# Kernel tuning notes

Hardware: AMD Instinct MI355X
Metric: run time of the kernel (lower is better)

The kernel has to match this reference:

```python
import jax, jax.numpy as jnp
import numpy as np

B, H, W, C = 8, 64, 64, 256
EPS = 1e-5


def unfold(img, k, p):
    # img: [B, C, Hh, Ww] -> patches [B, C, k*k, Hh*Ww] (torch.nn.Unfold layout)
    b, c, hh, ww = img.shape
    xp = jnp.pad(img, ((0, 0), (0, 0), (p, p), (p, p)))
    pats = jnp.stack([xp[:, :, i:i + hh, j:j + ww]
                      for i in range(k) for j in range(k)], axis=2)
    return pats.reshape(b, c, k * k, hh * ww)


def fold(cols, k, p, hh, ww):
    # cols: [B, C*k*k, hh*ww] -> scatter-add back to [B, C, hh, ww] (torch.nn.Fold)
    b = cols.shape[0]
    c = cols.shape[1] // (k * k)
    pt = cols.reshape(b, c, k, k, hh, ww)
    out = jnp.zeros((b, c, hh + 2 * p, ww + 2 * p), cols.dtype)
    for i in range(k):
        for j in range(k):
            out = out.at[:, :, i:i + hh, j:j + ww].add(pt[:, :, i, j])
    return out[:, :, p:p + hh, p:p + ww]


def maxpool(img, k, p):
    # same-size max pool, stride 1
    return jax.lax.reduce_window(img, -jnp.inf, jax.lax.max,
                                 (1, 1, k, k), (1, 1, 1, 1),
                                 [(0, 0), (0, 0), (p, p), (p, p)])


def setup_inputs() -> dict:
    key = jax.random.key(0)
    ks = jax.random.split(key, 4)
    x = jax.random.normal(ks[0], (B, H, W, C), dtype=jnp.float32)
    Wv = jax.random.normal(ks[1], (C, C), dtype=jnp.float32) * 0.02
    bv = jnp.zeros((C,), jnp.float32)
    Wa = jax.random.normal(ks[2], (C, 81), dtype=jnp.float32) * 0.02
    ba = jnp.zeros((81,), jnp.float32)
    Wfu = jax.random.normal(ks[3], (2 * C, C), dtype=jnp.float32) * 0.02
    bfu = jnp.zeros((C,), jnp.float32)
    gamma = jnp.ones((C,), jnp.float32)
    beta = jnp.zeros((C,), jnp.float32)
    return {"x": x, "Wv": Wv, "bv": bv, "Wa": Wa, "ba": ba,
            "Wfu": Wfu, "bfu": bfu, "gamma": gamma, "beta": beta}


def reference(x, Wv, bv, Wa, ba, Wfu, bfu, gamma, beta):
    b, h, w, c = x.shape
    x3 = x
    # 3x3 windowed attention branch (5x5 branch in source is dead code: its
    # result is overwritten by `x2 = relu(x)` before use).
    v = x @ Wv + bv                                # [B,H,W,C]
    v_img = jnp.transpose(v, (0, 3, 2, 1))         # [B,C,W,H] (H/W swap as in source)
    pats = unfold(v_img, 3, 1)                     # [B,C,9,W*H]
    v3 = jnp.transpose(pats, (0, 3, 2, 1))         # [B,HW,9,C]
    a = (x @ Wa + ba).reshape(b, h * w, 9, 9)
    a = jax.nn.softmax(a, axis=-1)
    y = jnp.einsum('lbpq,lbqc->lbpc'.replace('l', 'n'), a, v3)  # [B,HW,9,C]
    y = jnp.transpose(y, (0, 3, 2, 1)).reshape(b, c * 9, h * w)
    xf = fold(y, 3, 1, h, w)                       # [B,C,H,W]
    xf = jnp.transpose(xf, (0, 3, 2, 1))           # [B,W,H,C]
    xr = jax.nn.relu(xf)
    x_max = jnp.transpose(x3, (0, 3, 2, 1))        # [B,C,W,H]
    m1 = jnp.transpose(maxpool(x_max, 3, 1), (0, 3, 2, 1))  # [B,H,W,C]
    x1 = jax.nn.relu(xr + m1)
    x2 = jax.nn.relu(x1)
    m2 = jnp.transpose(maxpool(x_max, 5, 2), (0, 3, 2, 1))
    x2 = jax.nn.relu(x2 + m2)
    xfu = jnp.concatenate([x1, x2], axis=-1) @ Wfu + bfu
    xfu = jax.nn.relu(xfu)
    out = x3 + xfu                                 # [B,H,W,C]
    # BatchNorm2d (training mode: batch stats) applied on [B,C,W,H]
    img = jnp.transpose(out, (0, 3, 2, 1))
    mean = img.mean(axis=(0, 2, 3), keepdims=True)
    var = img.var(axis=(0, 2, 3), keepdims=True)
    imgn = (img - mean) * jax.lax.rsqrt(var + EPS)
    imgn = imgn * gamma[None, :, None, None] + beta[None, :, None, None]
    return jnp.transpose(imgn, (0, 2, 3, 1))       # [B,W,H,C]
```

## Files before the change

kernel.cpp:

```cpp
#include <hip/hip_runtime.h>
#include <math.h>

#define NLOC 32768
#define CH 256

typedef __attribute__((ext_vector_type(8))) short short8;
typedef __attribute__((ext_vector_type(4))) float floatx4;

__device__ inline unsigned short f2bf(float x) {
  union { float f; unsigned u; } c; c.f = x;
  unsigned r = c.u + 0x7FFFu + ((c.u >> 16) & 1u);
  return (unsigned short)(r >> 16);
}
__device__ inline float bflo(unsigned u) {
  union { unsigned u; float f; } c; c.u = u << 16; return c.f;
}
__device__ inline float bfhi(unsigned u) {
  union { unsigned u; float f; } c; c.u = u & 0xFFFF0000u; return c.f;
}

__device__ __forceinline__ void gl_lds16(const void* g, void* l) {
  __builtin_amdgcn_global_load_lds(
      (const __attribute__((address_space(1))) unsigned int*)g,
      (__attribute__((address_space(3))) unsigned int*)l, 16, 0, 0);
}

__global__ __launch_bounds__(64) void k_pack_w(
    const float* __restrict__ Wv, const float* __restrict__ Wa,
    const float* __restrict__ Wfu, unsigned short* __restrict__ wp) {
  int fid = blockIdx.x;
  int l = threadIdx.x;
  const float* W; int ldn, nvalid, nf, ks;
  if (fid < 128)      { W = Wv;  ldn = 256; nvalid = 256; nf = fid >> 3; ks = fid & 7; }
  else if (fid < 384) { int f = fid - 128; W = Wfu; ldn = 256; nvalid = 256; nf = f >> 4; ks = f & 15; }
  else                { int f = fid - 384; W = Wa;  ldn = 81;  nvalid = 81;  nf = f >> 3; ks = f & 7; }
  unsigned short* dst = wp + (size_t)fid * 512;
  int c = nf * 16 + (l & 15);
  int k0 = ks * 32 + (l >> 4) * 8;
  unsigned short u[8];
#pragma unroll
  for (int j = 0; j < 8; ++j)
    u[j] = (c < nvalid) ? f2bf(W[(size_t)(k0 + j) * ldn + c]) : (unsigned short)0;
  uint4 pk;
  pk.x = u[0] | ((unsigned)u[1] << 16);
  pk.y = u[2] | ((unsigned)u[3] << 16);
  pk.z = u[4] | ((unsigned)u[5] << 16);
  pk.w = u[6] | ((unsigned)u[7] << 16);
  *(uint4*)(dst + l * 8) = pk;
}

__global__ __launch_bounds__(256) void k_pool(
    const float* __restrict__ x, unsigned short* __restrict__ rm3,
    unsigned short* __restrict__ rm5, unsigned short* __restrict__ xb) {
  int tid = threadIdx.x;
  int loc = blockIdx.x * 4 + (tid >> 6);
  int beta = loc & 63;
  int c0 = (tid & 63) * 4;
  const float* base = x + ((size_t)loc - beta) * CH + c0;
  const float NI = -INFINITY;
  float4 r3 = {NI, NI, NI, NI}, r5, xv;
#pragma unroll
  for (int d = -1; d <= 1; ++d) {
    int bb = beta + d;
    if ((unsigned)bb >= 64u) continue;
    float4 f = *(const float4*)(base + (size_t)bb * CH);
    if (d == 0) xv = f;
    r3.x = fmaxf(r3.x, f.x); r3.y = fmaxf(r3.y, f.y);
    r3.z = fmaxf(r3.z, f.z); r3.w = fmaxf(r3.w, f.w);
  }
  r5 = r3;
#pragma unroll
  for (int d = -2; d <= 2; d += 4) {
    int bb = beta + d;
    if ((unsigned)bb >= 64u) continue;
    float4 f = *(const float4*)(base + (size_t)bb * CH);
    r5.x = fmaxf(r5.x, f.x); r5.y = fmaxf(r5.y, f.y);
    r5.z = fmaxf(r5.z, f.z); r5.w = fmaxf(r5.w, f.w);
  }
  size_t o = (size_t)loc * CH + c0;
  uint2 p3, p5, px;
  p3.x = f2bf(r3.x) | ((unsigned)f2bf(r3.y) << 16);
  p3.y = f2bf(r3.z) | ((unsigned)f2bf(r3.w) << 16);
  p5.x = f2bf(r5.x) | ((unsigned)f2bf(r5.y) << 16);
  p5.y = f2bf(r5.z) | ((unsigned)f2bf(r5.w) << 16);
  px.x = f2bf(xv.x) | ((unsigned)f2bf(xv.y) << 16);
  px.y = f2bf(xv.z) | ((unsigned)f2bf(xv.w) << 16);
  *(uint2*)(rm3 + o) = p3;
  *(uint2*)(rm5 + o) = p5;
  *(uint2*)(xb + o) = px;
}

__global__ __launch_bounds__(256) void k_gemm_v(
    const unsigned short* __restrict__ xb, const unsigned short* __restrict__ wvp,
    const float* __restrict__ bv, unsigned short* __restrict__ v) {
  __shared__ unsigned short sA[16 * 512];
  __shared__ unsigned short sB[16 * 512];
  int tid = threadIdx.x, lane = tid & 63, w = tid >> 6;
  int r0 = (blockIdx.x >> 1) * 128;
  int nc0 = (blockIdx.x & 1) * 128;
  int mh = w >> 1, nq = w & 1;
  floatx4 acc[4][4];
#pragma unroll
  for (int mt = 0; mt < 4; ++mt)
#pragma unroll
    for (int nf = 0; nf < 4; ++nf) acc[mt][nf] = (floatx4)(0.f);
  for (int kt = 0; kt < 4; ++kt) {
    int kk = kt * 64;
#pragma unroll
    for (int f = 0; f < 4; ++f) {
      int fa = w * 4 + f;
      int mt = fa >> 1, ks = fa & 1;
      const unsigned short* g = xb + (size_t)(r0 + mt * 16 + (lane & 15)) * CH
                                + kk + ks * 32 + (lane >> 4) * 8;
      gl_lds16(g, &sA[fa * 512]);
    }
#pragma unroll
    for (int f = 0; f < 4; ++f) {
      int fb = w * 4 + f;
      int nf = fb >> 1, ks = fb & 1;
      int nfg = (nc0 >> 4) + nf;
      int ksg = kt * 2 + ks;
      const unsigned short* g = wvp + ((size_t)nfg * 8 + ksg) * 512 + lane * 8;
      gl_lds16(g, &sB[fb * 512]);
    }
    __syncthreads();
#pragma unroll
    for (int ks = 0; ks < 2; ++ks) {
      short8 af[4], bf[4];
#pragma unroll
      for (int mt = 0; mt < 4; ++mt)
        af[mt] = *(const short8*)&sA[(((mh * 4 + mt) << 1) + ks) * 512 + lane * 8];
#pragma unroll
      for (int nf = 0; nf < 4; ++nf)
        bf[nf] = *(const short8*)&sB[(((nq * 4 + nf) << 1) + ks) * 512 + lane * 8];
#pragma unroll
      for (int mt = 0; mt < 4; ++mt)
#pragma unroll
        for (int nf = 0; nf < 4; ++nf)
          acc[mt][nf] = __builtin_amdgcn_mfma_f32_16x16x32_bf16(af[mt], bf[nf], acc[mt][nf], 0, 0, 0);
    }
    if (kt < 3) __syncthreads();
  }
#pragma unroll
  for (int nf = 0; nf < 4; ++nf) {
    int c = nc0 + nq * 64 + nf * 16 + (lane & 15);
    float bb = bv[c];
#pragma unroll
    for (int mt = 0; mt < 4; ++mt) {
      int crow = r0 + mh * 64 + mt * 16 + (lane >> 4) * 4;
#pragma unroll
      for (int i = 0; i < 4; ++i)
        v[(size_t)(crow + i) * CH + c] = f2bf(acc[mt][nf][i] + bb);
    }
  }
}

__global__ __launch_bounds__(256) void k_gemm_a(
    const unsigned short* __restrict__ xb, const unsigned short* __restrict__ wap,
    const float* __restrict__ ba, float* __restrict__ A) {
  __shared__ float lg[64][96];
  int tid = threadIdx.x, lane = tid & 63, w = tid >> 6;
  int mtile = blockIdx.x * 4 + w;
  int r0 = mtile * 16;
  floatx4 acc[6];
#pragma unroll
  for (int i = 0; i < 6; ++i) acc[i] = (floatx4)(0.f);
  const unsigned short* abase = xb + (size_t)(r0 + (lane & 15)) * CH + (lane >> 4) * 8;
  for (int ks = 0; ks < 8; ++ks) {
    short8 af = *(const short8*)(abase + ks * 32);
#pragma unroll
    for (int nf = 0; nf < 6; ++nf) {
      short8 bfr = *(const short8*)(wap + ((size_t)(nf * 8) + ks) * 512 + lane * 8);
      acc[nf] = __builtin_amdgcn_mfma_f32_16x16x32_bf16(af, bfr, acc[nf], 0, 0, 0);
    }
  }
  int lrow = w * 16 + (lane >> 4) * 4;
#pragma unroll
  for (int nf = 0; nf < 6; ++nf) {
    int c = nf * 16 + (lane & 15);
    float bb = (c < 81) ? ba[c] : 0.f;
#pragma unroll
    for (int i = 0; i < 4; ++i)
      lg[lrow + i][c] = acc[nf][i] + bb;
  }
  __syncthreads();
  int loc0 = blockIdx.x * 64;
  for (int it = 0; it < 3; ++it) {
    int idx = tid + it * 256;
    if (idx < 576) {
      int row = idx / 9, g = idx % 9;
      float vals[9];
#pragma unroll
      for (int q = 0; q < 9; ++q) vals[q] = lg[row][g * 9 + q];
      float m = vals[0];
#pragma unroll
      for (int q = 1; q < 9; ++q) m = fmaxf(m, vals[q]);
      float s = 0.f;
#pragma unroll
      for (int q = 0; q < 9; ++q) { vals[q] = __expf(vals[q] - m); s += vals[q]; }
      float inv = 1.f / s;
      float* o = A + (size_t)(loc0 + row) * 81 + g * 9;
#pragma unroll
      for (int q = 0; q < 9; ++q) o[q] = vals[q] * inv;
    }
  }
}

__global__ __launch_bounds__(256) void k_attn(
    const float* __restrict__ A, const unsigned short* __restrict__ v,
    const unsigned short* __restrict__ rm3, const unsigned short* __restrict__ rm5,
    unsigned short* __restrict__ cat) {
  __shared__ unsigned short vs[5 * 12 * CH];
  __shared__ float w5_s[8][25];
  float* a_sf = (float*)vs;
  int tid = threadIdx.x;
  int loc0 = blockIdx.x * 8;
  int b = loc0 >> 12, alpha = (loc0 >> 6) & 63, beta0 = loc0 & 63;
  for (int idx = tid; idx < 8 * 81; idx += 256) {
    int li = idx / 81, t = idx - li * 81;
    int ij = t / 9, i = ij / 3, j = ij % 3;
    int lh = beta0 + li + 1 - i;
    int lw = alpha + 1 - j;
    float val = 0.f;
    if ((unsigned)lh < 64u && (unsigned)lw < 64u)
      val = A[(size_t)(b * 4096 + lh * 64 + lw) * 81 + t];
    a_sf[li * 81 + t] = val;
  }
  __syncthreads();
  for (int idx = tid; idx < 200; idx += 256) {
    int li = idx / 25, o = idx - li * 25;
    int dh = o / 5 - 2, dw = o % 5 - 2;
    float s = 0.f;
    int jlo = dh < 0 ? -dh : 0, jhi = dh > 0 ? 2 - dh : 2;
    int ilo = dw < 0 ? -dw : 0, ihi = dw > 0 ? 2 - dw : 2;
    for (int j = jlo; j <= jhi; ++j)
      for (int i = ilo; i <= ihi; ++i)
        s += a_sf[li * 81 + (i * 3 + j) * 9 + ((i + dw) * 3 + (j + dh))];
    w5_s[li][o] = s;
  }
  __syncthreads();
  const unsigned short* vb = v + (size_t)b * 4096 * CH;
  for (int i = tid; i < 1920; i += 256) {
    int row = i / 384, rem = i - row * 384, col = rem >> 5, ch8 = rem & 31;
    int hv = alpha - 2 + row, wv = beta0 - 2 + col;
    uint4 val = {0u, 0u, 0u, 0u};
    if ((unsigned)hv < 64u && (unsigned)wv < 64u)
      val = *(const uint4*)(vb + (size_t)(hv * 64 + wv) * CH + ch8 * 8);
    *(uint4*)(vs + (size_t)(row * 12 + col) * CH + ch8 * 8) = val;
  }
  __syncthreads();
  int li = tid >> 5, tc = tid & 31, c0 = tc * 8;
  int beta = beta0 + li;
  float m1[8], m2[8];
#pragma unroll
  for (int q = 0; q < 8; ++q) { m1[q] = -INFINITY; m2[q] = -INFINITY; }
#pragma unroll
  for (int da = -2; da <= 2; ++da) {
    int aa = alpha + da;
    if ((unsigned)aa >= 64u) continue;
    size_t ro = (size_t)((b * 64 + aa) * 64 + beta) * CH + c0;
    uint4 p5 = *(const uint4*)(rm5 + ro);
    m2[0] = fmaxf(m2[0], bflo(p5.x)); m2[1] = fmaxf(m2[1], bfhi(p5.x));
    m2[2] = fmaxf(m2[2], bflo(p5.y)); m2[3] = fmaxf(m2[3], bfhi(p5.y));
    m2[4] = fmaxf(m2[4], bflo(p5.z)); m2[5] = fmaxf(m2[5], bfhi(p5.z));
    m2[6] = fmaxf(m2[6], bflo(p5.w)); m2[7] = fmaxf(m2[7], bfhi(p5.w));
    if (da >= -1 && da <= 1) {
      uint4 p3 = *(const uint4*)(rm3 + ro);
      m1[0] = fmaxf(m1[0], bflo(p3.x)); m1[1] = fmaxf(m1[1], bfhi(p3.x));
      m1[2] = fmaxf(m1[2], bflo(p3.y)); m1[3] = fmaxf(m1[3], bfhi(p3.y));
      m1[4] = fmaxf(m1[4], bflo(p3.z)); m1[5] = fmaxf(m1[5], bfhi(p3.z));
      m1[6] = fmaxf(m1[6], bflo(p3.w)); m1[7] = fmaxf(m1[7], bfhi(p3.w));
    }
  }
  float acc[8];
#pragma unroll
  for (int q = 0; q < 8; ++q) acc[q] = 0.f;
#pragma unroll
  for (int dh = 0; dh < 5; ++dh) {
#pragma unroll
    for (int dw = 0; dw < 5; ++dw) {
      float wgt = w5_s[li][dh * 5 + dw];
      uint4 pk = *(const uint4*)(vs + (size_t)(dh * 12 + li + dw) * CH + c0);
      acc[0] = fmaf(wgt, bflo(pk.x), acc[0]);
      acc[1] = fmaf(wgt, bfhi(pk.x), acc[1]);
      acc[2] = fmaf(wgt, bflo(pk.y), acc[2]);
      acc[3] = fmaf(wgt, bfhi(pk.y), acc[3]);
      acc[4] = fmaf(wgt, bflo(pk.z), acc[4]);
      acc[5] = fmaf(wgt, bfhi(pk.z), acc[5]);
      acc[6] = fmaf(wgt, bflo(pk.w), acc[6]);
      acc[7] = fmaf(wgt, bfhi(pk.w), acc[7]);
    }
  }
  unsigned short u1[8], u2[8];
#pragma unroll
  for (int q = 0; q < 8; ++q) {
    float x1v = fmaxf(fmaxf(acc[q], 0.f) + m1[q], 0.f);
    float x2v = fmaxf(x1v + m2[q], 0.f);
    u1[q] = f2bf(x1v);
    u2[q] = f2bf(x2v);
  }
  unsigned short* cp = cat + (size_t)(loc0 + li) * 512 + c0;
  uint4 pk1, pk2;
  pk1.x = u1[0] | ((unsigned)u1[1] << 16); pk1.y = u1[2] | ((unsigned)u1[3] << 16);
  pk1.z = u1[4] | ((unsigned)u1[5] << 16); pk1.w = u1[6] | ((unsigned)u1[7] << 16);
  pk2.x = u2[0] | ((unsigned)u2[1] << 16); pk2.y = u2[2] | ((unsigned)u2[3] << 16);
  pk2.z = u2[4] | ((unsigned)u2[5] << 16); pk2.w = u2[6] | ((unsigned)u2[7] << 16);
  *(uint4*)(cp) = pk1;
  *(uint4*)(cp + 256) = pk2;
}

__global__ __launch_bounds__(256) void k_fuse(
    const float* __restrict__ x, const unsigned short* __restrict__ cat,
    const unsigned short* __restrict__ wfp, const float* __restrict__ bfu,
    float* __restrict__ outp, float* __restrict__ sums) {
  __shared__ unsigned short sA[16 * 512];
  __shared__ unsigned short sB[16 * 512];
  __shared__ float bsum[512];
  int tid = threadIdx.x, lane = tid & 63, w = tid >> 6;
  for (int i = tid; i < 512; i += 256) bsum[i] = 0.f;
  int r0 = (blockIdx.x >> 1) * 128;
  int nc0 = (blockIdx.x & 1) * 128;
  int mh = w >> 1, nq = w & 1;
  floatx4 acc[4][4];
#pragma unroll
  for (int mt = 0; mt < 4; ++mt)
#pragma unroll
    for (int nf = 0; nf < 4; ++nf) acc[mt][nf] = (floatx4)(0.f);
  for (int kt = 0; kt < 8; ++kt) {
    int kk = kt * 64;
#pragma unroll
    for (int f = 0; f < 4; ++f) {
      int fa = w * 4 + f;
      int mt = fa >> 1, ks = fa & 1;
      const unsigned short* g = cat + (size_t)(r0 + mt * 16 + (lane & 15)) * 512
                                + kk + ks * 32 + (lane >> 4) * 8;
      gl_lds16(g, &sA[fa * 512]);
    }
#pragma unroll
    for (int f = 0; f < 4; ++f) {
      int fb = w * 4 + f;
      int nf = fb >> 1, ks = fb & 1;
      int nfg = (nc0 >> 4) + nf;
      int ksg = kt * 2 + ks;
      const unsigned short* g = wfp + ((size_t)nfg * 16 + ksg) * 512 + lane * 8;
      gl_lds16(g, &sB[fb * 512]);
    }
    __syncthreads();
#pragma unroll
    for (int ks = 0; ks < 2; ++ks) {
      short8 af[4], bf[4];
#pragma unroll
      for (int mt = 0; mt < 4; ++mt)
        af[mt] = *(const short8*)&sA[(((mh * 4 + mt) << 1) + ks) * 512 + lane * 8];
#pragma unroll
      for (int nf = 0; nf < 4; ++nf)
        bf[nf] = *(const short8*)&sB[(((nq * 4 + nf) << 1) + ks) * 512 + lane * 8];
#pragma unroll
      for (int mt = 0; mt < 4; ++mt)
#pragma unroll
        for (int nf = 0; nf < 4; ++nf)
          acc[mt][nf] = __builtin_amdgcn_mfma_f32_16x16x32_bf16(af[mt], bf[nf], acc[mt][nf], 0, 0, 0);
    }
    if (kt < 7) __syncthreads();
  }
#pragma unroll
  for (int nf = 0; nf < 4; ++nf) {
    int c = nc0 + nq * 64 + nf * 16 + (lane & 15);
    float bb = bfu[c];
    float s = 0.f, ss = 0.f;
#pragma unroll
    for (int mt = 0; mt < 4; ++mt) {
      int crow = r0 + mh * 64 + mt * 16 + (lane >> 4) * 4;
#pragma unroll
      for (int i = 0; i < 4; ++i) {
        int r = crow + i;
        float xv = x[(size_t)r * CH + c];
        float o = xv + fmaxf(acc[mt][nf][i] + bb, 0.f);
        int b_ = r >> 12, al = (r >> 6) & 63, be = r & 63;
        outp[((size_t)(b_ * 64 + be) * 64 + al) * CH + c] = o;
        s += o; ss += o * o;
      }
    }
    s += __shfl_xor(s, 16);  s += __shfl_xor(s, 32);
    ss += __shfl_xor(ss, 16); ss += __shfl_xor(ss, 32);
    if (lane < 16) {
      atomicAdd(&bsum[c & 255], s);
      atomicAdd(&bsum[256 + (c & 255)], ss);
    }
  }
  __syncthreads();
  for (int i = tid; i < 512; i += 256) atomicAdd(&sums[i], bsum[i]);
}

__global__ void k_bnprep(const float* __restrict__ sums,
                         const float* __restrict__ gamma,
                         const float* __restrict__ beta_,
                         float* __restrict__ sc) {
  int c = threadIdx.x;
  const float inv_n = 1.f / (float)NLOC;
  float mean = sums[c] * inv_n;
  float var = sums[256 + c] * inv_n - mean * mean;
  float scale = gamma[c] * rsqrtf(var + 1e-5f);
  sc[c] = scale;
  sc[256 + c] = beta_[c] - mean * scale;
}

__global__ __launch_bounds__(256) void k_bn(
    float* __restrict__ outp, const float* __restrict__ sc, int n4) {
  __shared__ float s[512];
  const int tid = threadIdx.x;
  for (int i = tid; i < 512; i += 256) s[i] = sc[i];
  __syncthreads();
  for (int i = blockIdx.x * 256 + tid; i < n4; i += gridDim.x * 256) {
    float4 val = ((float4*)outp)[i];
    int c0 = (i & 63) * 4;
    val.x = val.x * s[c0 + 0] + s[256 + c0 + 0];
    val.y = val.y * s[c0 + 1] + s[256 + c0 + 1];
    val.z = val.z * s[c0 + 2] + s[256 + c0 + 2];
    val.w = val.w * s[c0 + 3] + s[256 + c0 + 3];
    ((float4*)outp)[i] = val;
  }
}

extern "C" void kernel_launch(void* const* d_in, const int* in_sizes, int n_in,
                              void* d_out, int out_size, void* d_ws, size_t ws_size,
                              hipStream_t stream) {
  const float* x     = (const float*)d_in[0];
  const float* Wv    = (const float*)d_in[1];
  const float* bv    = (const float*)d_in[2];
  const float* Wa    = (const float*)d_in[3];
  const float* ba    = (const float*)d_in[4];
  const float* Wfu   = (const float*)d_in[5];
  const float* bfu   = (const float*)d_in[6];
  const float* gamma = (const float*)d_in[7];
  const float* beta_ = (const float*)d_in[8];
  float* out = (float*)d_out;

  float* sums = (float*)d_ws;
  float* sc   = sums + 512;
  unsigned short* wp   = (unsigned short*)(sc + 512);
  unsigned short* wvp  = wp;
  unsigned short* wfp  = wp + (size_t)128 * 512;
  unsigned short* wap  = wp + (size_t)384 * 512;
  unsigned short* vbuf = wp + (size_t)432 * 512;
  float* Abuf = (float*)(vbuf + (size_t)NLOC * CH);
  unsigned short* cat = (unsigned short*)(Abuf + (size_t)NLOC * 81);
  unsigned short* rm3 = cat + (size_t)NLOC * 512;
  unsigned short* rm5 = rm3 + (size_t)NLOC * CH;
  unsigned short* xb  = rm5 + (size_t)NLOC * CH;

  hipMemsetAsync(sums, 0, 512 * sizeof(float), stream);

  k_pack_w<<<432, 64, 0, stream>>>(Wv, Wa, Wfu, wp);
  k_pool<<<8192, 256, 0, stream>>>(x, rm3, rm5, xb);
  k_gemm_v<<<512, 256, 0, stream>>>(xb, wvp, bv, vbuf);
  k_gemm_a<<<512, 256, 0, stream>>>(xb, wap, ba, Abuf);
  k_attn<<<4096, 256, 0, stream>>>(Abuf, vbuf, rm3, rm5, cat);
  k_fuse<<<512, 256, 0, stream>>>(x, cat, wfp, bfu, out, sums);
  k_bnprep<<<1, 256, 0, stream>>>(sums, gamma, beta_, sc);
  k_bn<<<2048, 256, 0, stream>>>(out, sc, NLOC * CH / 4);
}
```

Before: 138.2 us.

## Store GEMM activations in MFMA fragment layout and halve row tile size

The producers (k_pool for xb, k_attn for cat) now write bf16 activations directly in the pre-swizzled 16x32 MFMA fragment layout. This makes each global_load_lds fetch a contiguous 1 KB fragment instead of 16 strided row segments, and k_gemm_a can read contiguous fragments as well. The v and fuse GEMMs also shrink the row tile from 128 to 64, doubling the grid to 1024 blocks for better occupancy and CU coverage. The cost is less reuse of the weight tile per block, so total B traffic rises, and the producers' stores become more scattered.

```diff
diff --git a/kernel.cpp b/kernel.cpp
--- a/kernel.cpp
+++ b/kernel.cpp
@@ -51,7 +51,7 @@
 
 __global__ __launch_bounds__(256) void k_pool(
     const float* __restrict__ x, unsigned short* __restrict__ rm3,
-    unsigned short* __restrict__ rm5, unsigned short* __restrict__ xb) {
+    unsigned short* __restrict__ rm5, unsigned short* __restrict__ xbf) {
   int tid = threadIdx.x;
   int loc = blockIdx.x * 4 + (tid >> 6);
   int beta = loc & 63;
@@ -87,54 +87,53 @@
   px.y = f2bf(xv.z) | ((unsigned)f2bf(xv.w) << 16);
   *(uint2*)(rm3 + o) = p3;
   *(uint2*)(rm5 + o) = p5;
-  *(uint2*)(xb + o) = px;
+  size_t fo = ((size_t)(loc >> 4) * 8 + (c0 >> 5)) * 512
+            + (((c0 >> 3) & 3) * 16 + (loc & 15)) * 8 + (c0 & 7);
+  *(uint2*)(xbf + fo) = px;
 }
 
 __global__ __launch_bounds__(256) void k_gemm_v(
-    const unsigned short* __restrict__ xb, const unsigned short* __restrict__ wvp,
+    const unsigned short* __restrict__ xbf, const unsigned short* __restrict__ wvp,
     const float* __restrict__ bv, unsigned short* __restrict__ v) {
-  __shared__ unsigned short sA[16 * 512];
+  __shared__ unsigned short sA[8 * 512];
   __shared__ unsigned short sB[16 * 512];
   int tid = threadIdx.x, lane = tid & 63, w = tid >> 6;
-  int r0 = (blockIdx.x >> 1) * 128;
+  int r0 = (blockIdx.x >> 1) * 64;
   int nc0 = (blockIdx.x & 1) * 128;
   int mh = w >> 1, nq = w & 1;
-  floatx4 acc[4][4];
-#pragma unroll
-  for (int mt = 0; mt < 4; ++mt)
+  int g16b = r0 >> 4;
+  floatx4 acc[2][4];
+#pragma unroll
+  for (int mt = 0; mt < 2; ++mt)
 #pragma unroll
     for (int nf = 0; nf < 4; ++nf) acc[mt][nf] = (floatx4)(0.f);
   for (int kt = 0; kt < 4; ++kt) {
-    int kk = kt * 64;
-#pragma unroll
-    for (int f = 0; f < 4; ++f) {
-      int fa = w * 4 + f;
-      int mt = fa >> 1, ks = fa & 1;
-      const unsigned short* g = xb + (size_t)(r0 + mt * 16 + (lane & 15)) * CH
-                                + kk + ks * 32 + (lane >> 4) * 8;
+#pragma unroll
+    for (int f = 0; f < 2; ++f) {
+      int fa = w * 2 + f;
+      int mt = fa >> 1, ksl = fa & 1;
+      const unsigned short* g = xbf + ((size_t)(g16b + mt) * 8 + kt * 2 + ksl) * 512 + lane * 8;
       gl_lds16(g, &sA[fa * 512]);
     }
 #pragma unroll
     for (int f = 0; f < 4; ++f) {
       int fb = w * 4 + f;
-      int nf = fb >> 1, ks = fb & 1;
-      int nfg = (nc0 >> 4) + nf;
-      int ksg = kt * 2 + ks;
-      const unsigned short* g = wvp + ((size_t)nfg * 8 + ksg) * 512 + lane * 8;
+      int nf = fb >> 1, ksl = fb & 1;
+      const unsigned short* g = wvp + ((size_t)((nc0 >> 4) + nf) * 8 + kt * 2 + ksl) * 512 + lane * 8;
       gl_lds16(g, &sB[fb * 512]);
     }
     __syncthreads();
 #pragma unroll
-    for (int ks = 0; ks < 2; ++ks) {
-      short8 af[4], bf[4];
-#pragma unroll
-      for (int mt = 0; mt < 4; ++mt)
-        af[mt] = *(const short8*)&sA[(((mh * 4 + mt) << 1) + ks) * 512 + lane * 8];
+    for (int ksl = 0; ksl < 2; ++ksl) {
+      short8 af[2], bf[4];
+#pragma unroll
+      for (int mt = 0; mt < 2; ++mt)
+        af[mt] = *(const short8*)&sA[(((mh * 2 + mt) << 1) + ksl) * 512 + lane * 8];
 #pragma unroll
       for (int nf = 0; nf < 4; ++nf)
-        bf[nf] = *(const short8*)&sB[(((nq * 4 + nf) << 1) + ks) * 512 + lane * 8];
-#pragma unroll
-      for (int mt = 0; mt < 4; ++mt)
+        bf[nf] = *(const short8*)&sB[(((nq * 4 + nf) << 1) + ksl) * 512 + lane * 8];
+#pragma unroll
+      for (int mt = 0; mt < 2; ++mt)
 #pragma unroll
         for (int nf = 0; nf < 4; ++nf)
           acc[mt][nf] = __builtin_amdgcn_mfma_f32_16x16x32_bf16(af[mt], bf[nf], acc[mt][nf], 0, 0, 0);
@@ -146,8 +145,8 @@
     int c = nc0 + nq * 64 + nf * 16 + (lane & 15);
     float bb = bv[c];
 #pragma unroll
-    for (int mt = 0; mt < 4; ++mt) {
-      int crow = r0 + mh * 64 + mt * 16 + (lane >> 4) * 4;
+    for (int mt = 0; mt < 2; ++mt) {
+      int crow = r0 + mh * 32 + mt * 16 + (lane >> 4) * 4;
 #pragma unroll
       for (int i = 0; i < 4; ++i)
         v[(size_t)(crow + i) * CH + c] = f2bf(acc[mt][nf][i] + bb);
@@ -156,18 +155,17 @@
 }
 
 __global__ __launch_bounds__(256) void k_gemm_a(
-    const unsigned short* __restrict__ xb, const unsigned short* __restrict__ wap,
+    const unsigned short* __restrict__ xbf, const unsigned short* __restrict__ wap,
     const float* __restrict__ ba, float* __restrict__ A) {
   __shared__ float lg[64][96];
   int tid = threadIdx.x, lane = tid & 63, w = tid >> 6;
   int mtile = blockIdx.x * 4 + w;
-  int r0 = mtile * 16;
   floatx4 acc[6];
 #pragma unroll
   for (int i = 0; i < 6; ++i) acc[i] = (floatx4)(0.f);
-  const unsigned short* abase = xb + (size_t)(r0 + (lane & 15)) * CH + (lane >> 4) * 8;
+  const unsigned short* abase = xbf + (size_t)mtile * 8 * 512 + lane * 8;
   for (int ks = 0; ks < 8; ++ks) {
-    short8 af = *(const short8*)(abase + ks * 32);
+    short8 af = *(const short8*)(abase + (size_t)ks * 512);
 #pragma unroll
     for (int nf = 0; nf < 6; ++nf) {
       short8 bfr = *(const short8*)(wap + ((size_t)(nf * 8) + ks) * 512 + lane * 8);
@@ -209,7 +207,7 @@
 __global__ __launch_bounds__(256) void k_attn(
     const float* __restrict__ A, const unsigned short* __restrict__ v,
     const unsigned short* __restrict__ rm3, const unsigned short* __restrict__ rm5,
-    unsigned short* __restrict__ cat) {
+    unsigned short* __restrict__ catf) {
   __shared__ unsigned short vs[5 * 12 * CH];
   __shared__ float w5_s[8][25];
   float* a_sf = (float*)vs;
@@ -299,64 +297,64 @@
     u1[q] = f2bf(x1v);
     u2[q] = f2bf(x2v);
   }
-  unsigned short* cp = cat + (size_t)(loc0 + li) * 512 + c0;
   uint4 pk1, pk2;
   pk1.x = u1[0] | ((unsigned)u1[1] << 16); pk1.y = u1[2] | ((unsigned)u1[3] << 16);
   pk1.z = u1[4] | ((unsigned)u1[5] << 16); pk1.w = u1[6] | ((unsigned)u1[7] << 16);
   pk2.x = u2[0] | ((unsigned)u2[1] << 16); pk2.y = u2[2] | ((unsigned)u2[3] << 16);
   pk2.z = u2[4] | ((unsigned)u2[5] << 16); pk2.w = u2[6] | ((unsigned)u2[7] << 16);
-  *(uint4*)(cp) = pk1;
-  *(uint4*)(cp + 256) = pk2;
+  int loc = loc0 + li;
+  int g16 = loc >> 4, row = loc & 15;
+  int ks1 = c0 >> 5, jg = (c0 >> 3) & 3;
+  size_t fb = ((size_t)g16 * 16 + ks1) * 512 + (jg * 16 + row) * 8;
+  *(uint4*)(catf + fb) = pk1;
+  *(uint4*)(catf + fb + (size_t)8 * 512) = pk2;
 }
 
 __global__ __launch_bounds__(256) void k_fuse(
-    const float* __restrict__ x, const unsigned short* __restrict__ cat,
+    const float* __restrict__ x, const unsigned short* __restrict__ catf,
     const unsigned short* __restrict__ wfp, const float* __restrict__ bfu,
     float* __restrict__ outp, float* __restrict__ sums) {
-  __shared__ unsigned short sA[16 * 512];
+  __shared__ unsigned short sA[8 * 512];
   __shared__ unsigned short sB[16 * 512];
   __shared__ float bsum[512];
   int tid = threadIdx.x, lane = tid & 63, w = tid >> 6;
   for (int i = tid; i < 512; i += 256) bsum[i] = 0.f;
-  int r0 = (blockIdx.x >> 1) * 128;
+  int r0 = (blockIdx.x >> 1) * 64;
   int nc0 = (blockIdx.x & 1) * 128;
   int mh = w >> 1, nq = w & 1;
-  floatx4 acc[4][4];
-#pragma unroll
-  for (int mt = 0; mt < 4; ++mt)
+  int g16b = r0 >> 4;
+  floatx4 acc[2][4];
+#pragma unroll
+  for (int mt = 0; mt < 2; ++mt)
 #pragma unroll
     for (int nf = 0; nf < 4; ++nf) acc[mt][nf] = (floatx4)(0.f);
   for (int kt = 0; kt < 8; ++kt) {
-    int kk = kt * 64;
-#pragma unroll
-    for (int f = 0; f < 4; ++f) {
-      int fa = w * 4 + f;
-      int mt = fa >> 1, ks = fa & 1;
-      const unsigned short* g = cat + (size_t)(r0 + mt * 16 + (lane & 15)) * 512
-                                + kk + ks * 32 + (lane >> 4) * 8;
+#pragma unroll
+    for (int f = 0; f < 2; ++f) {
+      int fa = w * 2 + f;
+      int mt = fa >> 1, ksl = fa & 1;
+      const unsigned short* g = catf + ((size_t)(g16b + mt) * 16 + kt * 2 + ksl) * 512 + lane * 8;
       gl_lds16(g, &sA[fa * 512]);
     }
 #pragma unroll
     for (int f = 0; f < 4; ++f) {
       int fb = w * 4 + f;
-      int nf = fb >> 1, ks = fb & 1;
-      int nfg = (nc0 >> 4) + nf;
-      int ksg = kt * 2 + ks;
-      const unsigned short* g = wfp + ((size_t)nfg * 16 + ksg) * 512 + lane * 8;
+      int nf = fb >> 1, ksl = fb & 1;
+      const unsigned short* g = wfp + ((size_t)((nc0 >> 4) + nf) * 16 + kt * 2 + ksl) * 512 + lane * 8;
       gl_lds16(g, &sB[fb * 512]);
     }
     __syncthreads();
 #pragma unroll
-    for (int ks = 0; ks < 2; ++ks) {
-      short8 af[4], bf[4];
-#pragma unroll
-      for (int mt = 0; mt < 4; ++mt)
-        af[mt] = *(const short8*)&sA[(((mh * 4 + mt) << 1) + ks) * 512 + lane * 8];
+    for (int ksl = 0; ksl < 2; ++ksl) {
+      short8 af[2], bf[4];
+#pragma unroll
+      for (int mt = 0; mt < 2; ++mt)
+        af[mt] = *(const short8*)&sA[(((mh * 2 + mt) << 1) + ksl) * 512 + lane * 8];
 #pragma unroll
       for (int nf = 0; nf < 4; ++nf)
-        bf[nf] = *(const short8*)&sB[(((nq * 4 + nf) << 1) + ks) * 512 + lane * 8];
-#pragma unroll
-      for (int mt = 0; mt < 4; ++mt)
+        bf[nf] = *(const short8*)&sB[(((nq * 4 + nf) << 1) + ksl) * 512 + lane * 8];
+#pragma unroll
+      for (int mt = 0; mt < 2; ++mt)
 #pragma unroll
         for (int nf = 0; nf < 4; ++nf)
           acc[mt][nf] = __builtin_amdgcn_mfma_f32_16x16x32_bf16(af[mt], bf[nf], acc[mt][nf], 0, 0, 0);
@@ -369,8 +367,8 @@
     float bb = bfu[c];
     float s = 0.f, ss = 0.f;
 #pragma unroll
-    for (int mt = 0; mt < 4; ++mt) {
-      int crow = r0 + mh * 64 + mt * 16 + (lane >> 4) * 4;
+    for (int mt = 0; mt < 2; ++mt) {
+      int crow = r0 + mh * 32 + mt * 16 + (lane >> 4) * 4;
 #pragma unroll
       for (int i = 0; i < 4; ++i) {
         int r = crow + i;
@@ -384,8 +382,8 @@
     s += __shfl_xor(s, 16);  s += __shfl_xor(s, 32);
     ss += __shfl_xor(ss, 16); ss += __shfl_xor(ss, 32);
     if (lane < 16) {
-      atomicAdd(&bsum[c & 255], s);
-      atomicAdd(&bsum[256 + (c & 255)], ss);
+      atomicAdd(&bsum[c], s);
+      atomicAdd(&bsum[256 + c], ss);
     }
   }
   __syncthreads();
@@ -444,19 +442,19 @@
   unsigned short* wap  = wp + (size_t)384 * 512;
   unsigned short* vbuf = wp + (size_t)432 * 512;
   float* Abuf = (float*)(vbuf + (size_t)NLOC * CH);
-  unsigned short* cat = (unsigned short*)(Abuf + (size_t)NLOC * 81);
-  unsigned short* rm3 = cat + (size_t)NLOC * 512;
+  unsigned short* catf = (unsigned short*)(Abuf + (size_t)NLOC * 81);
+  unsigned short* rm3 = catf + (size_t)NLOC * 512;
   unsigned short* rm5 = rm3 + (size_t)NLOC * CH;
-  unsigned short* xb  = rm5 + (size_t)NLOC * CH;
+  unsigned short* xbf = rm5 + (size_t)NLOC * CH;
 
   hipMemsetAsync(sums, 0, 512 * sizeof(float), stream);
 
   k_pack_w<<<432, 64, 0, stream>>>(Wv, Wa, Wfu, wp);
-  k_pool<<<8192, 256, 0, stream>>>(x, rm3, rm5, xb);
-  k_gemm_v<<<512, 256, 0, stream>>>(xb, wvp, bv, vbuf);
-  k_gemm_a<<<512, 256, 0, stream>>>(xb, wap, ba, Abuf);
-  k_attn<<<4096, 256, 0, stream>>>(Abuf, vbuf, rm3, rm5, cat);
-  k_fuse<<<512, 256, 0, stream>>>(x, cat, wfp, bfu, out, sums);
+  k_pool<<<8192, 256, 0, stream>>>(x, rm3, rm5, xbf);
+  k_gemm_v<<<1024, 256, 0, stream>>>(xbf, wvp, bv, vbuf);
+  k_gemm_a<<<512, 256, 0, stream>>>(xbf, wap, ba, Abuf);
+  k_attn<<<4096, 256, 0, stream>>>(Abuf, vbuf, rm3, rm5, catf);
+  k_fuse<<<1024, 256, 0, stream>>>(x, catf, wfp, bfu, out, sums);
   k_bnprep<<<1, 256, 0, stream>>>(sums, gamma, beta_, sc);
   k_bn<<<2048, 256, 0, stream>>>(out, sc, NLOC * CH / 4);
 }
```

After: 148.1 us. 7.1% more time.
